# Kernel tuning notes

Hardware: AMD Instinct MI355X
Metric: run time of the kernel (lower is better)

Reference implementation:

```python
import jax, jax.numpy as jnp
import numpy as np

B, H, N, C, E, D, L_OUT, LAYERS = 16, 64, 512, 3, 128, 32, 12, 2


def setup_inputs() -> dict:
    key = jax.random.key(0)
    ks = jax.random.split(key, 16)
    nrm = lambda k, s, sc=1.0: jax.random.normal(k, s, jnp.float32) * sc
    adj = jax.random.uniform(ks[0], (N, N), jnp.float32)
    adj = adj / adj.sum(axis=-1, keepdims=True)  # row-normalized prior adjacency
    return {
        "x_input": nrm(ks[1], (B, H, N, C)),
        "adj": adj,
        "Wf": nrm(ks[2], (3, E, 3 * C), 0.1),
        "Uf": nrm(ks[3], (3, E, E), 0.05),
        "bf": jnp.zeros((3, E), jnp.float32),
        "E1f": nrm(ks[4], (N, D)),
        "E2f": nrm(ks[5], (N, D)),
        "Wb": nrm(ks[6], (3, E, 3 * C), 0.1),
        "Ub": nrm(ks[7], (3, E, E), 0.05),
        "bb": jnp.zeros((3, E), jnp.float32),
        "E1b": nrm(ks[8], (N, D)),
        "E2b": nrm(ks[9], (N, D)),
        "dec_w": nrm(ks[10], (L_OUT, LAYERS, 2 * E), 0.05),  # Conv2d(layer_num->out_len, k=(1,2E)) squeezed
        "dec_b": jnp.zeros((L_OUT,), jnp.float32),
        "out_w": nrm(ks[11], (L_OUT, L_OUT), 0.1),  # 1x1 Conv2d squeezed
        "out_b": jnp.zeros((L_OUT,), jnp.float32),
    }


def _cell_step(c, xt, adj, A_dyn, W, U, b):
    # Graph-coupled GRU cell (IBNCell): xt [B,C,N], c [B,E,N].
    msg = jnp.concatenate(
        [xt,
         jnp.einsum('bcn,nm->bcm', xt, adj),      # prior-graph message passing
         jnp.einsum('bcn,nm->bcm', xt, A_dyn)],   # learned dynamic-graph message passing
        axis=1)  # [B, 3C, N]
    gx = jnp.einsum('goc,bcn->gbon', W, msg)  # 3 stacked gate projections
    r = jax.nn.sigmoid(gx[0] + jnp.einsum('oe,ben->bon', U[0], c) + b[0][:, None])
    u = jax.nn.sigmoid(gx[1] + jnp.einsum('oe,ben->bon', U[1], c) + b[1][:, None])
    g = jnp.tanh(gx[2] + jnp.einsum('oe,ben->bon', U[2], r * c) + b[2][:, None])
    return u * c + (1.0 - u) * g


def _forward(x_input, adj, Wf, Uf, bf, E1f, E2f, Wb, Ub, bb, E1b, E2b, dec_w, dec_b, out_w, out_b):
    # torch: x_input.transpose(-3,-1).transpose(-2,-1) -> [B,C,H,N]; scan layout [H,B,C,N]
    xs = jnp.transpose(x_input, (1, 0, 3, 2))
    A_f = jax.nn.softmax(jax.nn.relu(E1f @ E2f.T), axis=-1)  # dynamic adjacency, fwd cell
    A_b = jax.nn.softmax(jax.nn.relu(E1b @ E2b.T), axis=-1)  # dynamic adjacency, back cell
    c0 = jnp.zeros((xs.shape[1], Wf.shape[1], xs.shape[3]), xs.dtype)  # [B,E,N]

    def step_f(c, xt):
        cn = _cell_step(c, xt, adj, A_f, Wf, Uf, bf)
        return cn, None

    # Output only depends on the last timestep of the bidirectional concat:
    # forward branch -> final state after H steps; backward branch (after flip)
    # at t=H-1 -> its FIRST step (input x[H-1]). Dead per-step outputs elided.
    h_fwd, _ = jax.lax.scan(step_f, c0, xs)
    h_back0 = _cell_step(c0, xs[-1], adj, A_b, Wb, Ub, bb)
    last_ht = jnp.concatenate([h_fwd, h_back0], axis=1)  # [B, 2E, N]

    lt = jnp.transpose(last_ht, (0, 2, 1))  # [B, N, 2E]
    # layer loop z>0 is a no-op on current_layer_output -> final_result repeats last_ht
    final = jnp.broadcast_to(lt[:, None], (lt.shape[0], LAYERS, lt.shape[1], lt.shape[2]))
    h = jnp.einsum('blne,ole->bon', final, dec_w) + dec_b[:, None]  # decoder conv (1,2E)
    return jnp.einsum('oi,bin->bon', out_w, h) + out_b[:, None]  # 1x1 output conv -> [B,L_OUT,N]


def reference(x_input, adj, Wf, Uf, bf, E1f, E2f, Wb, Ub, bb, E1b, E2b, dec_w, dec_b, out_w, out_b):
    return _forward(x_input, adj, Wf, Uf, bf, E1f, E2f, Wb, Ub, bb, E1b, E2b, dec_w, dec_b, out_w, out_b)
```

## Files before the change

### kernel.cpp

```cpp
#include <hip/hip_runtime.h>


typedef _Float16 half8_t __attribute__((ext_vector_type(8)));
typedef __fp16 fp16x2_t __attribute__((ext_vector_type(2)));
typedef float float4_t __attribute__((ext_vector_type(4)));

#define PIN(x) asm volatile("" : "+v"(x))

__device__ __forceinline__ float exp2_(float x) { return __builtin_amdgcn_exp2f(x); }
__device__ __forceinline__ float rcp_(float x) { return __builtin_amdgcn_rcpf(x); }

__global__ __launch_bounds__(256) void prep_kernel(
    const float* __restrict__ E1f, const float* __restrict__ E2f,
    const float* __restrict__ E1b, const float* __restrict__ E2b,
    const float* __restrict__ x, const float* __restrict__ Wf,
    const float* __restrict__ Uf, const float* __restrict__ bf,
    const float* __restrict__ Wb, const float* __restrict__ bb,
    _Float16* __restrict__ AfR, _Float16* __restrict__ AbR,
    _Float16* __restrict__ xT16, _Float16* __restrict__ ufrag,
    _Float16* __restrict__ wbfrag) {
  int bid = blockIdx.x;
  int tid = threadIdx.x;
  if (bid >= 1160) {
    int bid2 = bid - 1160;
    int b = bid2 >> 6, t = bid2 & 63;
    const float2* xp = (const float2*)(x + (size_t)(b * 64 + t) * 1536);
    float2 f0 = xp[tid * 3], f1 = xp[tid * 3 + 1], f2 = xp[tid * 3 + 2];
    _Float16* dst = xT16 + (size_t)(b * 64 + t) * 1536;
    int n0_ = tid * 2;
    dst[n0_] = (_Float16)f0.x;
    dst[512 + n0_] = (_Float16)f0.y;
    dst[1024 + n0_] = (_Float16)f1.x;
    dst[n0_ + 1] = (_Float16)f1.y;
    dst[512 + n0_ + 1] = (_Float16)f2.x;
    dst[1024 + n0_ + 1] = (_Float16)f2.y;
    return;
  }
  if (bid >= 1144) {
    int r2 = bid - 1144;
    int gi = 1 + (r2 & 1);
    int og = r2 >> 1;
    float scl = (gi == 2) ? 2.8853902f : -1.4426950f;
    for (int e = tid; e < 512; e += 256) {
      int lane = e >> 3, j = e & 7;
      int o = og * 16 + (lane & 15);
      int q = (lane >> 4) * 8 + j;
      float v = (q < 9) ? Wb[gi * 1152 + o * 9 + q]
                        : (q == 9 ? bb[gi * 128 + o] : 0.f);
      wbfrag[r2 * 512 + e] = (_Float16)(v * scl);
    }
    return;
  }
  if (bid >= 1024) {
    int r = bid - 1024;
    int kb = r % 5;
    int gi = (r / 5) % 3;
    int og = r / 15;
    float scl = (gi == 2) ? 2.8853902f : -1.4426950f;
    for (int e = tid; e < 512; e += 256) {
      int lane = e >> 3, j = e & 7;
      int o = og * 16 + (lane & 15);
      int q4 = lane >> 4;
      float v;
      if (kb < 4) {
        v = Uf[gi * 16384 + o * 128 + kb * 32 + q4 * 8 + j];
      } else {
        int q = q4 * 8 + j;
        v = (q < 9) ? Wf[gi * 1152 + o * 9 + q]
                    : (q == 9 ? bf[gi * 128 + o] : 0.f);
      }
      ufrag[r * 512 + e] = (_Float16)(v * scl);
    }
    return;
  }
  int which = bid >> 9;
  int row = bid & 511;
  const float* E1 = which ? E1b : E1f;
  const float* E2 = which ? E2b : E2f;
  _Float16* A = which ? AbR : AfR;
  __shared__ float e1s[32];
  __shared__ float red[256];
  if (tid < 32) e1s[tid] = E1[row * 32 + tid];
  __syncthreads();
  float s[2];
#pragma unroll
  for (int h = 0; h < 2; ++h) {
    int m = tid + h * 256;
    const float4* e2 = (const float4*)(E2 + m * 32);
    float acc = 0.f;
#pragma unroll
    for (int d4 = 0; d4 < 8; ++d4) {
      float4 v = e2[d4];
      acc = fmaf(v.x, e1s[d4 * 4 + 0], acc);
      acc = fmaf(v.y, e1s[d4 * 4 + 1], acc);
      acc = fmaf(v.z, e1s[d4 * 4 + 2], acc);
      acc = fmaf(v.w, e1s[d4 * 4 + 3], acc);
    }
    s[h] = fmaxf(acc, 0.f);
  }
  red[tid] = fmaxf(s[0], s[1]);
  __syncthreads();
  for (int off = 128; off > 0; off >>= 1) {
    if (tid < off) red[tid] = fmaxf(red[tid], red[tid + off]);
    __syncthreads();
  }
  float mx = red[0];
  __syncthreads();
  float e0 = __expf(s[0] - mx), e1v = __expf(s[1] - mx);
  red[tid] = e0 + e1v;
  __syncthreads();
  for (int off = 128; off > 0; off >>= 1) {
    if (tid < off) red[tid] += red[tid + off];
    __syncthreads();
  }
  float inv = rcp_(red[0]);
  A[(size_t)row * 512 + tid] = (_Float16)(e0 * inv);
  A[(size_t)row * 512 + tid + 256] = (_Float16)(e1v * inv);
}

__global__ __launch_bounds__(256) void transpose_kernel(
    const float* __restrict__ adj, const _Float16* __restrict__ AfR,
    const _Float16* __restrict__ AbR, _Float16* __restrict__ adjT,
    _Float16* __restrict__ AfT, _Float16* __restrict__ AbT) {
  __shared__ _Float16 T[64][65];
  int bid = blockIdx.x;
  int mat = bid >> 6;
  int tile = bid & 63;
  int tr = tile >> 3, tc = tile & 7;
  int t = threadIdx.x;
  int r = t >> 2, cb = (t & 3) * 16;
  if (mat == 0) {
    const float* s = adj + (size_t)(tr * 64 + r) * 512 + tc * 64 + cb;
#pragma unroll
    for (int i = 0; i < 16; ++i) T[r][cb + i] = (_Float16)s[i];
  } else {
    const _Float16* s =
        (mat == 1 ? AfR : AbR) + (size_t)(tr * 64 + r) * 512 + tc * 64 + cb;
#pragma unroll
    for (int i = 0; i < 16; ++i) T[r][cb + i] = s[i];
  }
  __syncthreads();
  _Float16* d = (mat == 0 ? adjT : mat == 1 ? AfT : AbT) +
                (size_t)(tc * 64 + r) * 512 + tr * 64 + cb;
#pragma unroll
  for (int i = 0; i < 16; ++i) d[i] = T[cb + i][r];
}

__global__ __launch_bounds__(256, 4) void msg_kernel(
    const _Float16* __restrict__ xT16, const _Float16* __restrict__ adjT,
    const _Float16* __restrict__ AfT, const _Float16* __restrict__ AbT,
    _Float16* __restrict__ msg16, _Float16* __restrict__ msgb16) {
  __shared__ __align__(8) _Float16 Sst[512 * 12];
  int tid = threadIdx.x;
  int t = blockIdx.x >> 4;
  int n0g = (blockIdx.x & 15) * 32;
  int lane = tid & 63, og = tid >> 6;
  int l15 = lane & 15, q4 = lane >> 4, q0 = q4 * 8;
  int nt = og & 1, mat = og >> 1;
  bool is63 = (t == 63);
  bool doAb = is63 && (mat == 0);

  const _Float16* Bmat = mat ? AfT : adjT;
  int n = n0g + nt * 16 + l15;

  const float4_t zero4 = {0.f, 0.f, 0.f, 0.f};
  float4_t acc[3], accb[3];
#pragma unroll
  for (int mt = 0; mt < 3; ++mt) { acc[mt] = zero4; accb[mt] = zero4; }

  for (int kb = 0; kb < 16; ++kb) {
    half8_t b0 = *(const half8_t*)&Bmat[(size_t)n * 512 + kb * 32 + q0];
    half8_t b2;
    if (doAb) b2 = *(const half8_t*)&AbT[(size_t)n * 512 + kb * 32 + q0];
#pragma unroll
    for (int mt = 0; mt < 3; ++mt) {
      int m = mt * 16 + l15;
      int bm = (m * 21846) >> 16;
      int cm = m - bm * 3;
      half8_t a = *(const half8_t*)
          &xT16[((size_t)(bm * 64 + t) * 3 + cm) * 512 + kb * 32 + q0];
      acc[mt] = __builtin_amdgcn_mfma_f32_16x16x32_f16(a, b0, acc[mt], 0, 0, 0);
      if (doAb)
        accb[mt] = __builtin_amdgcn_mfma_f32_16x16x32_f16(a, b2, accb[mt], 0, 0, 0);
    }
  }

  for (int i = tid; i < 512; i += 256) {
    int tb = i >> 5, nl = i & 31;
    int nn = n0g + nl;
    _Float16* row = &Sst[i * 12];
#pragma unroll
    for (int c = 0; c < 3; ++c)
      row[c] = xT16[((size_t)(tb * 64 + t) * 3 + c) * 512 + nn];
    row[9] = (_Float16)1.f;
    row[10] = (_Float16)0.f;
    row[11] = (_Float16)0.f;
  }
#pragma unroll
  for (int mt = 0; mt < 3; ++mt)
#pragma unroll
    for (int r = 0; r < 4; ++r) {
      int m = mt * 16 + q4 * 4 + r;
      int tb = (m * 21846) >> 16;
      int c = m - tb * 3;
      Sst[((size_t)tb * 32 + nt * 16 + l15) * 12 + 3 + mat * 3 + c] =
          (_Float16)acc[mt][r];
    }
  __syncthreads();
  for (int i = tid; i < 512; i += 256) {
    int tb = i >> 5, nl = i & 31;
    const uint2* s = (const uint2*)&Sst[i * 12];
    uint2* dst = (uint2*)&msg16[((size_t)(t * 16 + tb) * 512 + n0g + nl) * 12];
    dst[0] = s[0]; dst[1] = s[1]; dst[2] = s[2];
  }
  if (is63) {
    __syncthreads();
    if (mat == 0) {
#pragma unroll
      for (int mt = 0; mt < 3; ++mt)
#pragma unroll
        for (int r = 0; r < 4; ++r) {
          int m = mt * 16 + q4 * 4 + r;
          int tb = (m * 21846) >> 16;
          int c = m - tb * 3;
          Sst[((size_t)tb * 32 + nt * 16 + l15) * 12 + 6 + c] = (_Float16)accb[mt][r];
        }
    }
    __syncthreads();
    for (int i = tid; i < 512; i += 256) {
      int tb = i >> 5, nl = i & 31;
      const uint2* s = (const uint2*)&Sst[i * 12];
      uint2* dst = (uint2*)&msgb16[((size_t)tb * 512 + n0g + nl) * 12];
      dst[0] = s[0]; dst[1] = s[1]; dst[2] = s[2];
    }
  }
}

__global__ __launch_bounds__(512, 4) void rec_kernel(
    const _Float16* __restrict__ msg16, const _Float16* __restrict__ msgb16,
    const _Float16* __restrict__ ufrag, const _Float16* __restrict__ wbfrag,
    const float* __restrict__ dec_w, const float* __restrict__ dec_b,
    const float* __restrict__ out_w, const float* __restrict__ out_b,
    float* __restrict__ out) {
  __shared__ __align__(16) _Float16 Cbuf[2048];
  __shared__ __align__(16) _Float16 Gbuf[2048];
  __shared__ float hf_lds[128 * 16];
  __shared__ float hb_lds[128 * 16];
  __shared__ float hdec_lds[12 * 16];
  int tid = threadIdx.x, bid = blockIdx.x;
  int b = bid >> 5;
  int nt = bid & 31;
  int n0 = nt * 16;
  int lane = tid & 63, og = tid >> 6;
  int l15 = lane & 15, q4 = lane >> 4;

  half8_t afrag[3][5];
#pragma unroll
  for (int gi = 0; gi < 3; ++gi)
#pragma unroll
    for (int kb = 0; kb < 5; ++kb) {
      afrag[gi][kb] = *(const half8_t*)
          &ufrag[(size_t)(((og * 3 + gi) * 5 + kb) * 512) + lane * 8];
      PIN(afrag[gi][kb]);
    }

  if (tid < 256) {
    uint4 z; z.x = z.y = z.z = z.w = 0;
    ((uint4*)Cbuf)[tid] = z;
  }
  float cr[4] = {0.f, 0.f, 0.f, 0.f};

  const float4_t zero4 = {0.f, 0.f, 0.f, 0.f};
  union H4U { fp16x2_t h2[2]; unsigned long long u; };
  union U16 { uint4 u4; half8_t h8; };
  unsigned odd = q4 & 1;
  const size_t tstride = (size_t)16 * 512 * 24;
  const char* mrow = (const char*)msg16 + ((size_t)(b * 512 + n0 + l15)) * 24;

  U16 bu;
  {
    uint4 lo = *(const uint4*)mrow;
    uint2 hi = *(const uint2*)(mrow + 16);
    bu.u4.x = odd ? hi.x : lo.x;
    bu.u4.y = odd ? hi.y : lo.y;
    bu.u4.z = odd ? 0u : lo.z;
    bu.u4.w = odd ? 0u : lo.w;
  }
  half8_t bm = bu.h8;

  int kb_w = og >> 1;
  int lane_w = ((og & 1) * 2 + (q4 >> 1)) * 16 + l15;
  int j0 = (q4 & 1) * 4;
  __syncthreads();

  for (int t = 0; t < 64; ++t) {
    int tn = (t < 63) ? t + 1 : 63;
    const char* p = mrow + (size_t)tn * tstride;
    uint4 lo = *(const uint4*)p;
    uint2 hi = *(const uint2*)(p + 16);

    half8_t cf[4];
#pragma unroll
    for (int kb = 0; kb < 4; ++kb)
      cf[kb] = *(const half8_t*)&Cbuf[(kb * 64 + lane) * 8];

    float4_t accr = zero4, accu = zero4;
#pragma unroll
    for (int kb = 0; kb < 4; ++kb) {
      accr = __builtin_amdgcn_mfma_f32_16x16x32_f16(afrag[0][kb], cf[kb], accr, 0, 0, 0);
      accu = __builtin_amdgcn_mfma_f32_16x16x32_f16(afrag[1][kb], cf[kb], accu, 0, 0, 0);
    }
    accr = __builtin_amdgcn_mfma_f32_16x16x32_f16(afrag[0][4], bm, accr, 0, 0, 0);
    accu = __builtin_amdgcn_mfma_f32_16x16x32_f16(afrag[1][4], bm, accu, 0, 0, 0);
    float4_t accg = __builtin_amdgcn_mfma_f32_16x16x32_f16(afrag[2][4], bm, zero4, 0, 0, 0);

    {
      float rc0 = rcp_(1.f + exp2_(accr[0])) * cr[0];
      float rc1 = rcp_(1.f + exp2_(accr[1])) * cr[1];
      float rc2 = rcp_(1.f + exp2_(accr[2])) * cr[2];
      float rc3 = rcp_(1.f + exp2_(accr[3])) * cr[3];
      H4U v;
      v.h2[0] = __builtin_amdgcn_cvt_pkrtz(rc0, rc1);
      v.h2[1] = __builtin_amdgcn_cvt_pkrtz(rc2, rc3);
      *(unsigned long long*)&Gbuf[(kb_w * 64 + lane_w) * 8 + j0] = v.u;
    }
    __syncthreads();

    half8_t gf[4];
#pragma unroll
    for (int kb = 0; kb < 4; ++kb)
      gf[kb] = *(const half8_t*)&Gbuf[(kb * 64 + lane) * 8];
#pragma unroll
    for (int kb = 0; kb < 4; ++kb)
      accg = __builtin_amdgcn_mfma_f32_16x16x32_f16(afrag[2][kb], gf[kb], accg, 0, 0, 0);

    {
      H4U v;
      float cn[4];
#pragma unroll
      for (int r = 0; r < 4; ++r) {
        float uu = rcp_(1.f + exp2_(accu[r]));
        float gg = fmaf(-2.f, rcp_(exp2_(accg[r]) + 1.f), 1.f);
        cn[r] = fmaf(uu, cr[r] - gg, gg);
        cr[r] = cn[r];
      }
      v.h2[0] = __builtin_amdgcn_cvt_pkrtz(cn[0], cn[1]);
      v.h2[1] = __builtin_amdgcn_cvt_pkrtz(cn[2], cn[3]);
      *(unsigned long long*)&Cbuf[(kb_w * 64 + lane_w) * 8 + j0] = v.u;
    }
    __syncthreads();

    bu.u4.x = odd ? hi.x : lo.x;
    bu.u4.y = odd ? hi.y : lo.y;
    bu.u4.z = odd ? 0u : lo.z;
    bu.u4.w = odd ? 0u : lo.w;
    bm = bu.h8;
  }

  {
    const char* p = (const char*)msgb16 + ((size_t)(b * 512 + n0 + l15)) * 24;
    uint4 lo = *(const uint4*)p;
    uint2 hi = *(const uint2*)(p + 16);
    U16 bb2;
    bb2.u4.x = odd ? hi.x : lo.x;
    bb2.u4.y = odd ? hi.y : lo.y;
    bb2.u4.z = odd ? 0u : lo.z;
    bb2.u4.w = odd ? 0u : lo.w;
    half8_t au_f = *(const half8_t*)&wbfrag[(size_t)((og * 2 + 0) * 512) + lane * 8];
    half8_t ag_f = *(const half8_t*)&wbfrag[(size_t)((og * 2 + 1) * 512) + lane * 8];
    float4_t au = __builtin_amdgcn_mfma_f32_16x16x32_f16(au_f, bb2.h8, zero4, 0, 0, 0);
    float4_t ag = __builtin_amdgcn_mfma_f32_16x16x32_f16(ag_f, bb2.h8, zero4, 0, 0, 0);
#pragma unroll
    for (int r = 0; r < 4; ++r) {
      int row = og * 16 + q4 * 4 + r;
      float uu = rcp_(1.f + exp2_(au[r]));
      float gg = fmaf(-2.f, rcp_(exp2_(ag[r]) + 1.f), 1.f);
      hb_lds[row * 16 + l15] = (1.f - uu) * gg;
      hf_lds[row * 16 + l15] = cr[r];
    }
  }
  __syncthreads();

  if (tid < 192) {
    int i = tid >> 4, cc = tid & 15;
    const float* dwa = dec_w + (size_t)i * 512;
    const float* dwb = dwa + 256;
    float hd = dec_b[i];
    for (int e = 0; e < 128; ++e) {
      hd = fmaf(dwa[e] + dwb[e], hf_lds[e * 16 + cc], hd);
      hd = fmaf(dwa[128 + e] + dwb[128 + e], hb_lds[e * 16 + cc], hd);
    }
    hdec_lds[i * 16 + cc] = hd;
  }
  __syncthreads();
  if (tid < 192) {
    int o = tid >> 4, cc = tid & 15;
    float v = out_b[o];
#pragma unroll
    for (int i = 0; i < 12; ++i) v = fmaf(out_w[o * 12 + i], hdec_lds[i * 16 + cc], v);
    out[((size_t)(b * 12 + o)) * 512 + n0 + cc] = v;
  }
}

extern "C" void kernel_launch(void* const* d_in, const int* in_sizes, int n_in,
                              void* d_out, int out_size, void* d_ws, size_t ws_size,
                              hipStream_t stream) {
  (void)in_sizes; (void)n_in; (void)out_size; (void)ws_size;
  const float* x     = (const float*)d_in[0];
  const float* adj   = (const float*)d_in[1];
  const float* Wf    = (const float*)d_in[2];
  const float* Uf    = (const float*)d_in[3];
  const float* bf    = (const float*)d_in[4];
  const float* E1f   = (const float*)d_in[5];
  const float* E2f   = (const float*)d_in[6];
  const float* Wb    = (const float*)d_in[7];
  const float* bb    = (const float*)d_in[9];
  const float* E1b   = (const float*)d_in[10];
  const float* E2b   = (const float*)d_in[11];
  const float* dec_w = (const float*)d_in[12];
  const float* dec_b = (const float*)d_in[13];
  const float* out_w = (const float*)d_in[14];
  const float* out_b = (const float*)d_in[15];

  _Float16* h      = (_Float16*)d_ws;
  _Float16* adjT   = h;
  _Float16* AfT    = h + 262144;
  _Float16* AbT    = h + 524288;
  _Float16* ufrag  = h + 786432;
  _Float16* wbfrag = h + 847872;
  _Float16* xT16   = h + 856064;
  _Float16* msg16  = h + 2428928;
  _Float16* msgb16 = h + 8720384;
  _Float16* AfR    = h + 8818688;
  _Float16* AbR    = h + 9080832;

  prep_kernel<<<2184, 256, 0, stream>>>(E1f, E2f, E1b, E2b, x, Wf, Uf, bf,
                                        Wb, bb, AfR, AbR, xT16, ufrag, wbfrag);
  transpose_kernel<<<192, 256, 0, stream>>>(adj, AfR, AbR, adjT, AfT, AbT);
  msg_kernel<<<1024, 256, 0, stream>>>(xT16, adjT, AfT, AbT, msg16, msgb16);
  rec_kernel<<<512, 512, 0, stream>>>(msg16, msgb16, ufrag, wbfrag,
                                      dec_w, dec_b, out_w, out_b, (float*)d_out);
}
```

Baseline: 216.4 us.

## Preload per-tile message slices into LDS and split MFMA accumulation chains

The message kernel now writes its output in a slice-major layout (per batch/node tile, all 64 timesteps contiguous), with the ninth channel split into a separate buffer. The recurrence kernel bulk-loads all 64 timesteps of its slice into LDS up front, so the serial loop no longer issues a global load each step. The recurrent MFMA chains are also split into two independent accumulators to shorten the dependency chain, and the update-gate sigmoid is hoisted before the barrier. In exchange it uses about 33 KB more LDS per block, adds a prologue load, and aliases the adjacency scratch buffers onto the message buffer.

```diff
diff --git a/kernel.cpp b/kernel.cpp
--- a/kernel.cpp
+++ b/kernel.cpp
@@ -149,11 +149,14 @@
 __global__ __launch_bounds__(256, 4) void msg_kernel(
     const _Float16* __restrict__ xT16, const _Float16* __restrict__ adjT,
     const _Float16* __restrict__ AfT, const _Float16* __restrict__ AbT,
-    _Float16* __restrict__ msg16, _Float16* __restrict__ msgb16) {
-  __shared__ __align__(8) _Float16 Sst[512 * 12];
+    _Float16* __restrict__ msgF, _Float16* __restrict__ msgF2,
+    _Float16* __restrict__ msgbF, _Float16* __restrict__ msgb2) {
+  __shared__ __align__(16) _Float16 Sst[32 * 16 * 8];
+  __shared__ __align__(16) _Float16 Sf2[32 * 16];
   int tid = threadIdx.x;
   int t = blockIdx.x >> 4;
-  int n0g = (blockIdx.x & 15) * 32;
+  int nc = blockIdx.x & 15;
+  int n0g = nc * 32;
   int lane = tid & 63, og = tid >> 6;
   int l15 = lane & 15, q4 = lane >> 4, q0 = q4 * 8;
   int nt = og & 1, mat = og >> 1;
@@ -186,15 +189,12 @@
   }
 
   for (int i = tid; i < 512; i += 256) {
-    int tb = i >> 5, nl = i & 31;
-    int nn = n0g + nl;
-    _Float16* row = &Sst[i * 12];
+    int tb = i >> 5, r = i & 31, nt2 = r >> 4, cl = r & 15;
+    int nn = n0g + nt2 * 16 + cl;
+    _Float16* row = &Sst[((tb * 2 + nt2) * 16 + cl) * 8];
 #pragma unroll
     for (int c = 0; c < 3; ++c)
       row[c] = xT16[((size_t)(tb * 64 + t) * 3 + c) * 512 + nn];
-    row[9] = (_Float16)1.f;
-    row[10] = (_Float16)0.f;
-    row[11] = (_Float16)0.f;
   }
 #pragma unroll
   for (int mt = 0; mt < 3; ++mt)
@@ -203,15 +203,23 @@
       int m = mt * 16 + q4 * 4 + r;
       int tb = (m * 21846) >> 16;
       int c = m - tb * 3;
-      Sst[((size_t)tb * 32 + nt * 16 + l15) * 12 + 3 + mat * 3 + c] =
-          (_Float16)acc[mt][r];
+      int sl = tb * 2 + nt;
+      if (mat == 0) Sst[(sl * 16 + l15) * 8 + 3 + c] = (_Float16)acc[mt][r];
+      else if (c < 2) Sst[(sl * 16 + l15) * 8 + 6 + c] = (_Float16)acc[mt][r];
+      else Sf2[sl * 16 + l15] = (_Float16)acc[mt][r];
     }
   __syncthreads();
   for (int i = tid; i < 512; i += 256) {
-    int tb = i >> 5, nl = i & 31;
-    const uint2* s = (const uint2*)&Sst[i * 12];
-    uint2* dst = (uint2*)&msg16[((size_t)(t * 16 + tb) * 512 + n0g + nl) * 12];
-    dst[0] = s[0]; dst[1] = s[1]; dst[2] = s[2];
+    int sl = i >> 4, u = i & 15;
+    int tb = sl >> 1, nt2 = sl & 1;
+    size_t slice = (size_t)tb * 32 + nc * 2 + nt2;
+    ((uint4*)msgF)[(slice * 64 + t) * 16 + u] = ((const uint4*)Sst)[i];
+  }
+  if (tid < 64) {
+    int sl = tid >> 1, h = tid & 1;
+    int tb = sl >> 1, nt2 = sl & 1;
+    size_t slice = (size_t)tb * 32 + nc * 2 + nt2;
+    ((uint4*)msgF2)[(slice * 64 + t) * 2 + h] = ((const uint4*)Sf2)[sl * 2 + h];
   }
   if (is63) {
     __syncthreads();
@@ -223,25 +231,35 @@
           int m = mt * 16 + q4 * 4 + r;
           int tb = (m * 21846) >> 16;
           int c = m - tb * 3;
-          Sst[((size_t)tb * 32 + nt * 16 + l15) * 12 + 6 + c] = (_Float16)accb[mt][r];
+          int sl = tb * 2 + nt;
+          if (c < 2) Sst[(sl * 16 + l15) * 8 + 6 + c] = (_Float16)accb[mt][r];
+          else Sf2[sl * 16 + l15] = (_Float16)accb[mt][r];
         }
     }
     __syncthreads();
     for (int i = tid; i < 512; i += 256) {
-      int tb = i >> 5, nl = i & 31;
-      const uint2* s = (const uint2*)&Sst[i * 12];
-      uint2* dst = (uint2*)&msgb16[((size_t)tb * 512 + n0g + nl) * 12];
-      dst[0] = s[0]; dst[1] = s[1]; dst[2] = s[2];
+      int sl = i >> 4, u = i & 15;
+      int tb = sl >> 1, nt2 = sl & 1;
+      size_t slice = (size_t)tb * 32 + nc * 2 + nt2;
+      ((uint4*)msgbF)[slice * 16 + u] = ((const uint4*)Sst)[i];
+    }
+    if (tid < 64) {
+      int sl = tid >> 1, h = tid & 1;
+      int tb = sl >> 1, nt2 = sl & 1;
+      size_t slice = (size_t)tb * 32 + nc * 2 + nt2;
+      ((uint4*)msgb2)[slice * 2 + h] = ((const uint4*)Sf2)[sl * 2 + h];
     }
   }
 }
 
 __global__ __launch_bounds__(512, 4) void rec_kernel(
-    const _Float16* __restrict__ msg16, const _Float16* __restrict__ msgb16,
+    const _Float16* __restrict__ msgF, const _Float16* __restrict__ msgF2,
+    const _Float16* __restrict__ msgbF, const _Float16* __restrict__ msgb2,
     const _Float16* __restrict__ ufrag, const _Float16* __restrict__ wbfrag,
     const float* __restrict__ dec_w, const float* __restrict__ dec_b,
     const float* __restrict__ out_w, const float* __restrict__ out_b,
     float* __restrict__ out) {
+  __shared__ __align__(16) _Float16 Bmsg[65 * 256];
   __shared__ __align__(16) _Float16 Cbuf[2048];
   __shared__ __align__(16) _Float16 Gbuf[2048];
   __shared__ float hf_lds[128 * 16];
@@ -253,6 +271,7 @@
   int n0 = nt * 16;
   int lane = tid & 63, og = tid >> 6;
   int l15 = lane & 15, q4 = lane >> 4;
+  size_t slice = (size_t)b * 32 + nt;
 
   half8_t afrag[3][5];
 #pragma unroll
@@ -264,65 +283,81 @@
       PIN(afrag[gi][kb]);
     }
 
+  {
+    const uint4* src = (const uint4*)msgF + slice * 64 * 16;
+    uint4 z; z.x = z.y = z.z = z.w = 0;
+    for (int f = tid; f < 1024; f += 512) {
+      int t = f >> 4, u = f & 15;
+      ((uint4*)Bmsg)[t * 32 + u] = src[f];
+      ((uint4*)Bmsg)[t * 32 + 16 + u] = z;
+    }
+  }
+  if (tid < 16) {
+    ((uint4*)Bmsg)[64 * 32 + tid] = ((const uint4*)msgbF)[slice * 16 + tid];
+    ((uint4*)Bmsg)[64 * 32 + 16 + tid] = uint4{0, 0, 0, 0};
+  }
   if (tid < 256) {
     uint4 z; z.x = z.y = z.z = z.w = 0;
     ((uint4*)Cbuf)[tid] = z;
   }
+  __syncthreads();
+  {
+    const _Float16* f2p = msgF2 + slice * 64 * 16;
+    for (int f = tid; f < 1024; f += 512) {
+      int t = f >> 4, l = f & 15;
+      _Float16* d = &Bmsg[(t * 32 + 16 + l) * 8];
+      d[0] = f2p[t * 16 + l];
+      d[1] = (_Float16)1.f;
+    }
+    if (tid < 16) {
+      _Float16* d = &Bmsg[(64 * 32 + 16 + tid) * 8];
+      d[0] = msgb2[slice * 16 + tid];
+      d[1] = (_Float16)1.f;
+    }
+  }
   float cr[4] = {0.f, 0.f, 0.f, 0.f};
 
   const float4_t zero4 = {0.f, 0.f, 0.f, 0.f};
   union H4U { fp16x2_t h2[2]; unsigned long long u; };
-  union U16 { uint4 u4; half8_t h8; };
-  unsigned odd = q4 & 1;
-  const size_t tstride = (size_t)16 * 512 * 24;
-  const char* mrow = (const char*)msg16 + ((size_t)(b * 512 + n0 + l15)) * 24;
-
-  U16 bu;
-  {
-    uint4 lo = *(const uint4*)mrow;
-    uint2 hi = *(const uint2*)(mrow + 16);
-    bu.u4.x = odd ? hi.x : lo.x;
-    bu.u4.y = odd ? hi.y : lo.y;
-    bu.u4.z = odd ? 0u : lo.z;
-    bu.u4.w = odd ? 0u : lo.w;
-  }
-  half8_t bm = bu.h8;
-
   int kb_w = og >> 1;
   int lane_w = ((og & 1) * 2 + (q4 >> 1)) * 16 + l15;
   int j0 = (q4 & 1) * 4;
+  int bm_off = ((lane & 31)) * 8;
   __syncthreads();
 
   for (int t = 0; t < 64; ++t) {
-    int tn = (t < 63) ? t + 1 : 63;
-    const char* p = mrow + (size_t)tn * tstride;
-    uint4 lo = *(const uint4*)p;
-    uint2 hi = *(const uint2*)(p + 16);
-
+    half8_t bm = *(const half8_t*)&Bmsg[t * 256 + bm_off];
     half8_t cf[4];
 #pragma unroll
     for (int kb = 0; kb < 4; ++kb)
       cf[kb] = *(const half8_t*)&Cbuf[(kb * 64 + lane) * 8];
 
-    float4_t accr = zero4, accu = zero4;
-#pragma unroll
-    for (int kb = 0; kb < 4; ++kb) {
-      accr = __builtin_amdgcn_mfma_f32_16x16x32_f16(afrag[0][kb], cf[kb], accr, 0, 0, 0);
-      accu = __builtin_amdgcn_mfma_f32_16x16x32_f16(afrag[1][kb], cf[kb], accu, 0, 0, 0);
-    }
-    accr = __builtin_amdgcn_mfma_f32_16x16x32_f16(afrag[0][4], bm, accr, 0, 0, 0);
-    accu = __builtin_amdgcn_mfma_f32_16x16x32_f16(afrag[1][4], bm, accu, 0, 0, 0);
-    float4_t accg = __builtin_amdgcn_mfma_f32_16x16x32_f16(afrag[2][4], bm, zero4, 0, 0, 0);
-
+    float4_t accr1 = __builtin_amdgcn_mfma_f32_16x16x32_f16(afrag[0][0], cf[0], zero4, 0, 0, 0);
+    float4_t accu1 = __builtin_amdgcn_mfma_f32_16x16x32_f16(afrag[1][0], cf[0], zero4, 0, 0, 0);
+    float4_t accr2 = __builtin_amdgcn_mfma_f32_16x16x32_f16(afrag[0][4], bm, zero4, 0, 0, 0);
+    float4_t accu2 = __builtin_amdgcn_mfma_f32_16x16x32_f16(afrag[1][4], bm, zero4, 0, 0, 0);
+    float4_t accg_p = __builtin_amdgcn_mfma_f32_16x16x32_f16(afrag[2][4], bm, zero4, 0, 0, 0);
+    accr1 = __builtin_amdgcn_mfma_f32_16x16x32_f16(afrag[0][1], cf[1], accr1, 0, 0, 0);
+    accu1 = __builtin_amdgcn_mfma_f32_16x16x32_f16(afrag[1][1], cf[1], accu1, 0, 0, 0);
+    accr2 = __builtin_amdgcn_mfma_f32_16x16x32_f16(afrag[0][2], cf[2], accr2, 0, 0, 0);
+    accu2 = __builtin_amdgcn_mfma_f32_16x16x32_f16(afrag[1][2], cf[2], accu2, 0, 0, 0);
+    accr2 = __builtin_amdgcn_mfma_f32_16x16x32_f16(afrag[0][3], cf[3], accr2, 0, 0, 0);
+    accu2 = __builtin_amdgcn_mfma_f32_16x16x32_f16(afrag[1][3], cf[3], accu2, 0, 0, 0);
+
+    float uu[4];
     {
-      float rc0 = rcp_(1.f + exp2_(accr[0])) * cr[0];
-      float rc1 = rcp_(1.f + exp2_(accr[1])) * cr[1];
-      float rc2 = rcp_(1.f + exp2_(accr[2])) * cr[2];
-      float rc3 = rcp_(1.f + exp2_(accr[3])) * cr[3];
+      float4_t accr = accr1 + accr2;
+      float4_t accu = accu1 + accu2;
       H4U v;
-      v.h2[0] = __builtin_amdgcn_cvt_pkrtz(rc0, rc1);
-      v.h2[1] = __builtin_amdgcn_cvt_pkrtz(rc2, rc3);
+#pragma unroll
+      for (int r = 0; r < 2; ++r) {
+        float a = rcp_(1.f + exp2_(accr[2 * r])) * cr[2 * r];
+        float bq = rcp_(1.f + exp2_(accr[2 * r + 1])) * cr[2 * r + 1];
+        v.h2[r] = __builtin_amdgcn_cvt_pkrtz(a, bq);
+      }
       *(unsigned long long*)&Gbuf[(kb_w * 64 + lane_w) * 8 + j0] = v.u;
+#pragma unroll
+      for (int r = 0; r < 4; ++r) uu[r] = rcp_(1.f + exp2_(accu[r]));
     }
     __syncthreads();
 
@@ -330,18 +365,19 @@
 #pragma unroll
     for (int kb = 0; kb < 4; ++kb)
       gf[kb] = *(const half8_t*)&Gbuf[(kb * 64 + lane) * 8];
-#pragma unroll
-    for (int kb = 0; kb < 4; ++kb)
-      accg = __builtin_amdgcn_mfma_f32_16x16x32_f16(afrag[2][kb], gf[kb], accg, 0, 0, 0);
+    float4_t accg1 = __builtin_amdgcn_mfma_f32_16x16x32_f16(afrag[2][0], gf[0], accg_p, 0, 0, 0);
+    float4_t accg2 = __builtin_amdgcn_mfma_f32_16x16x32_f16(afrag[2][2], gf[2], zero4, 0, 0, 0);
+    accg1 = __builtin_amdgcn_mfma_f32_16x16x32_f16(afrag[2][1], gf[1], accg1, 0, 0, 0);
+    accg2 = __builtin_amdgcn_mfma_f32_16x16x32_f16(afrag[2][3], gf[3], accg2, 0, 0, 0);
 
     {
+      float4_t accg = accg1 + accg2;
       H4U v;
       float cn[4];
 #pragma unroll
       for (int r = 0; r < 4; ++r) {
-        float uu = rcp_(1.f + exp2_(accu[r]));
         float gg = fmaf(-2.f, rcp_(exp2_(accg[r]) + 1.f), 1.f);
-        cn[r] = fmaf(uu, cr[r] - gg, gg);
+        cn[r] = fmaf(uu[r], cr[r] - gg, gg);
         cr[r] = cn[r];
       }
       v.h2[0] = __builtin_amdgcn_cvt_pkrtz(cn[0], cn[1]);
@@ -349,33 +385,20 @@
       *(unsigned long long*)&Cbuf[(kb_w * 64 + lane_w) * 8 + j0] = v.u;
     }
     __syncthreads();
-
-    bu.u4.x = odd ? hi.x : lo.x;
-    bu.u4.y = odd ? hi.y : lo.y;
-    bu.u4.z = odd ? 0u : lo.z;
-    bu.u4.w = odd ? 0u : lo.w;
-    bm = bu.h8;
   }
 
   {
-    const char* p = (const char*)msgb16 + ((size_t)(b * 512 + n0 + l15)) * 24;
-    uint4 lo = *(const uint4*)p;
-    uint2 hi = *(const uint2*)(p + 16);
-    U16 bb2;
-    bb2.u4.x = odd ? hi.x : lo.x;
-    bb2.u4.y = odd ? hi.y : lo.y;
-    bb2.u4.z = odd ? 0u : lo.z;
-    bb2.u4.w = odd ? 0u : lo.w;
+    half8_t bbk = *(const half8_t*)&Bmsg[64 * 256 + bm_off];
     half8_t au_f = *(const half8_t*)&wbfrag[(size_t)((og * 2 + 0) * 512) + lane * 8];
     half8_t ag_f = *(const half8_t*)&wbfrag[(size_t)((og * 2 + 1) * 512) + lane * 8];
-    float4_t au = __builtin_amdgcn_mfma_f32_16x16x32_f16(au_f, bb2.h8, zero4, 0, 0, 0);
-    float4_t ag = __builtin_amdgcn_mfma_f32_16x16x32_f16(ag_f, bb2.h8, zero4, 0, 0, 0);
+    float4_t au = __builtin_amdgcn_mfma_f32_16x16x32_f16(au_f, bbk, zero4, 0, 0, 0);
+    float4_t ag = __builtin_amdgcn_mfma_f32_16x16x32_f16(ag_f, bbk, zero4, 0, 0, 0);
 #pragma unroll
     for (int r = 0; r < 4; ++r) {
       int row = og * 16 + q4 * 4 + r;
-      float uu = rcp_(1.f + exp2_(au[r]));
+      float uu2 = rcp_(1.f + exp2_(au[r]));
       float gg = fmaf(-2.f, rcp_(exp2_(ag[r]) + 1.f), 1.f);
-      hb_lds[row * 16 + l15] = (1.f - uu) * gg;
+      hb_lds[row * 16 + l15] = (1.f - uu2) * gg;
       hf_lds[row * 16 + l15] = cr[r];
     }
   }
@@ -429,15 +452,18 @@
   _Float16* ufrag  = h + 786432;
   _Float16* wbfrag = h + 847872;
   _Float16* xT16   = h + 856064;
-  _Float16* msg16  = h + 2428928;
-  _Float16* msgb16 = h + 8720384;
-  _Float16* AfR    = h + 8818688;
-  _Float16* AbR    = h + 9080832;
+  _Float16* msgF   = h + 2428928;
+  _Float16* msgF2  = h + 6623232;
+  _Float16* msgbF  = h + 7147520;
+  _Float16* msgb2  = h + 7213056;
+  _Float16* AfR    = msgF;
+  _Float16* AbR    = msgF + 262144;
 
   prep_kernel<<<2184, 256, 0, stream>>>(E1f, E2f, E1b, E2b, x, Wf, Uf, bf,
                                         Wb, bb, AfR, AbR, xT16, ufrag, wbfrag);
   transpose_kernel<<<192, 256, 0, stream>>>(adj, AfR, AbR, adjT, AfT, AbT);
-  msg_kernel<<<1024, 256, 0, stream>>>(xT16, adjT, AfT, AbT, msg16, msgb16);
-  rec_kernel<<<512, 512, 0, stream>>>(msg16, msgb16, ufrag, wbfrag,
+  msg_kernel<<<1024, 256, 0, stream>>>(xT16, adjT, AfT, AbT, msgF, msgF2,
+                                       msgbF, msgb2);
+  rec_kernel<<<512, 512, 0, stream>>>(msgF, msgF2, msgbF, msgb2, ufrag, wbfrag,
                                       dec_w, dec_b, out_w, out_b, (float*)d_out);
 }
```

Measured after the change: 217.9 us. No clear change (+0.7%).
